# Optimization experiments

Hardware: AMD Instinct MI355X
Metric: run time of the kernel (lower is better)

Reference implementation:

```python
import jax, jax.numpy as jnp
from jax import lax
import numpy as np

# ---- config (repo globals, scaled to a 112x112 feature map of a 448 image) ----
IMG, FEAT = 448, 112
PSTRIDE = IMG // FEAT  # 4 pixels per feature cell
RATIOS = [(16, 16), (12, 20), (20, 12),
          (24, 24), (20, 28), (28, 20),
          (32, 32), (24, 40), (40, 24), (28, 40), (40, 28), (28, 36), (36, 28)]
GROUPS = [(0, 3), (3, 6), (6, 13)]   # ratio groups per NMS scale
N_LIST = [2, 3, 2]
IOU_THRESHS = [0.25, 0.25, 0.25]
BATCH = 256
WINDOW_NUMS = [(FEAT - rh + 1) * (FEAT - rw + 1) for rh, rw in RATIOS]
TOTAL = sum(WINDOW_NUMS)             # 96981
PROPOSALN = sum(N_LIST)              # 7


def _coordinates():
    # Mirrors ComputeCoordinate: box = [x0,y0,x1,y1] in pixels, lefttop clipped to 0.
    parts = []
    for rh, rw in RATIOS:
        nr, nc = FEAT - rh + 1, FEAT - rw + 1
        xi = np.repeat(np.arange(nr), nc).astype(np.float32)
        yi = np.tile(np.arange(nc), nr).astype(np.float32)
        x0 = xi * PSTRIDE - 1.0
        y0 = yi * PSTRIDE - 1.0
        x1 = x0 + rh * PSTRIDE
        y1 = y0 + rw * PSTRIDE
        x0 = np.maximum(x0, 0.0)
        y0 = np.maximum(y0, 0.0)
        parts.append(np.stack([x0, y0, x1, y1], 1))
    return np.concatenate(parts, 0).astype(np.float32)  # (TOTAL, 4)


def setup_inputs() -> dict:
    key = jax.random.key(0)
    x = jax.random.normal(key, (BATCH, 1, FEAT, FEAT), jnp.float32)
    coords = jnp.asarray(_coordinates())
    return {"x": x, "coords": coords, "proposalN": PROPOSALN}


def _nms(scores, coords, n_pick, thresh):
    # Greedy NMS: repeatedly take best-scoring alive window, suppress IoU > thresh.
    # If everything is suppressed before n_pick picks, repeat the last pick (repo behavior).
    areas = (coords[:, 2] - coords[:, 0] + 1.0) * (coords[:, 3] - coords[:, 1] + 1.0)

    def step(state, _):
        alive, last = state
        any_alive = jnp.any(alive)
        idx = jnp.where(any_alive,
                        jnp.argmax(jnp.where(alive, scores, -jnp.inf)).astype(jnp.int32),
                        last)
        box = coords[idx]
        lt = jnp.maximum(coords[:, :2], box[:2])
        rb = jnp.minimum(coords[:, 2:], box[2:])
        w = rb[:, 0] - lt[:, 0] + 1.0
        h = rb[:, 1] - lt[:, 1] + 1.0
        inter = jnp.where((w < 0) | (h < 0), 0.0, w * h)
        iou = inter / (areas + areas[idx] - inter)
        keep = (alive & (iou <= thresh)).at[idx].set(False)
        return (jnp.where(any_alive, keep, alive), idx), idx

    init = (jnp.ones(scores.shape[0], bool), jnp.int32(0))
    return lax.scan(step, init, None, length=n_pick)[1]  # (n_pick,) int32


def _forward(x, coords):
    B = x.shape[0]
    # multiscale sliding-window average scores (AvgPool2d, stride 1, VALID)
    avgs = [lax.reduce_window(x, 0.0, lax.add, (1, 1, rh, rw), (1, 1, 1, 1), 'VALID')
            .reshape(B, -1) / float(rh * rw) for rh, rw in RATIOS]
    all_scores = jnp.concatenate(avgs, 1)  # (B, TOTAL)

    idx_parts = []
    for j, (g0, g1) in enumerate(GROUPS):
        s0 = int(sum(WINDOW_NUMS[:g0]))
        s1 = int(sum(WINDOW_NUMS[:g1]))
        cd = coords[s0:s1]
        nms_j = lambda s, cd=cd, j=j: _nms(s, cd, N_LIST[j], IOU_THRESHS[j])
        picks = jax.vmap(nms_j)(all_scores[:, s0:s1])  # (B, N_LIST[j])
        idx_parts.append(picks + s0)
    proposalN_indices = jnp.concatenate(idx_parts, 1)  # (B, PROPOSALN)
    proposalN_windows_scores = jnp.take_along_axis(all_scores, proposalN_indices, 1)
    window_scores = all_scores  # reshape(batch, -1) of all_scores
    return proposalN_indices, proposalN_windows_scores, window_scores


def reference(x, coords, proposalN):
    assert proposalN == PROPOSALN
    return _forward(x, coords)
```

## Files before the change

kernel.cpp:

```cpp
#include <hip/hip_runtime.h>
#include <math.h>
#include <limits.h>

namespace {
constexpr int kFeat = 112;
constexpr int kBatch = 256;
constexpr int kTotal = 96981;
constexpr int kStride = 116;
constexpr int kNT = 512;
constexpr int kRH[13] = {16,12,20,24,20,28,32,24,40,28,40,28,36};
constexpr int kRW[13] = {16,20,12,24,28,20,32,40,24,40,28,36,28};
constexpr int kOff[13] = {0,9409,18802,28195,36116,44021,51926,58487,64984,71481,77686,83891,90436};
constexpr int kNQY[13] = {25,24,26,23,22,24,21,19,23,19,22,20,22};
constexpr int kNQ[13]  = {2425,2424,2418,2047,2046,2040,1701,1691,1679,1615,1606,1700,1694};
constexpr int kNB[13]  = {38,38,38,32,32,32,27,27,27,26,26,27,27};
constexpr int kNBMax = 187;

constexpr int nb_sum(int RB, int RE) {
  int s = 0;
  for (int r = RB; r < RE; ++r) s += kNB[r];
  return s;
}
}

__device__ __forceinline__ float* pad_score(float* sat, int e) {
  return sat + (e / 3) * kStride + 113 + (e % 3);
}
__device__ __forceinline__ unsigned char* pad_local(float* sat, int e) {
  const int i = 4 * kNBMax + e;
  const int r = i / 12;
  return (unsigned char*)sat + r * (kStride * 4) + 113 * 4 + (i - r * 12);
}

struct NmsShared {
  float rs[kNT / 64];
  int   ri[kNT / 64];
  float shS; int shI;
  float pX0[3], pY0[3], pX1[3], pY1[3], pA[3];
};

__device__ __forceinline__ void block_argmax(float s, int i, NmsShared* ns) {
  __syncthreads();
#pragma unroll
  for (int off = 32; off > 0; off >>= 1) {
    const float s2 = __shfl_down(s, off, 64);
    const int   i2 = __shfl_down(i, off, 64);
    if (s2 > s || (s2 == s && i2 < i)) { s = s2; i = i2; }
  }
  const int wave = threadIdx.x >> 6;
  if ((threadIdx.x & 63) == 0) { ns->rs[wave] = s; ns->ri[wave] = i; }
  __syncthreads();
  if (threadIdx.x == 0) {
    float bs = ns->rs[0]; int bi = ns->ri[0];
#pragma unroll
    for (int w = 1; w < kNT / 64; ++w)
      if (ns->rs[w] > bs || (ns->rs[w] == bs && ns->ri[w] < bi)) { bs = ns->rs[w]; bi = ns->ri[w]; }
    ns->shS = bs; ns->shI = bi;
  }
  __syncthreads();
}

__device__ void build_sat(const float* __restrict__ xb, float* __restrict__ sat) {
  const int tid = threadIdx.x;
  for (int j = tid; j < kStride; j += kNT) sat[j] = 0.f;
  for (int r = tid; r < 113; r += kNT) sat[r * kStride] = 0.f;
  const float4* x4 = (const float4*)xb;
  for (int i = tid; i < (kFeat * kFeat) / 4; i += kNT) {
    const float4 v = x4[i];
    const int r = i / (kFeat / 4);
    const int c = (i - r * (kFeat / 4)) * 4;
    float* dst = sat + (r + 1) * kStride + c + 1;
    dst[0] = v.x; dst[1] = v.y; dst[2] = v.z; dst[3] = v.w;
  }
  __syncthreads();
  const int wave = tid >> 6, lane = tid & 63;
  for (int r = 1 + wave; r <= kFeat; r += kNT / 64) {
    float* row = sat + r * kStride;
    float v = row[1 + lane];
#pragma unroll
    for (int d = 1; d < 64; d <<= 1) { const float u = __shfl_up(v, d, 64); if (lane >= d) v += u; }
    row[1 + lane] = v;
    const float tot = __shfl(v, 63, 64);
    const int c = 65 + lane;
    float w = (c <= kFeat) ? row[c] : 0.f;
#pragma unroll
    for (int d = 1; d < 64; d <<= 1) { const float u = __shfl_up(w, d, 64); if (lane >= d) w += u; }
    if (c <= kFeat) row[c] = w + tot;
  }
  __syncthreads();
  const int seg = tid / kFeat;
  const int col = tid - seg * kFeat + 1;
  if (tid < 4 * kFeat) {
    const int r0 = seg * 28 + 1;
    float s = 0.f;
    for (int r = r0; r < r0 + 28; ++r) { s += sat[r * kStride + col]; sat[r * kStride + col] = s; }
  }
  __syncthreads();
  float off = 0.f;
  if (tid < 4 * kFeat && seg > 0) {
#pragma unroll
    for (int s2 = 1; s2 <= 3; ++s2)
      if (s2 <= seg) off += sat[(28 * s2) * kStride + col];
  }
  __syncthreads();
  if (tid < 4 * kFeat && seg > 0) {
    const int r0 = seg * 28 + 1;
    for (int r = r0; r < r0 + 28; ++r) sat[r * kStride + col] += off;
  }
  __syncthreads();
}

template<int RB, int RE>
__device__ __forceinline__ void decode_geom(int pi, float& x0, float& y0,
                                            float& x1, float& y1, float& a) {
  x0 = 0.f; y0 = 0.f; x1 = 0.f; y1 = 0.f; a = 0.f;
#pragma unroll
  for (int rr = RB; rr < RE; ++rr) {
    const int nr = kFeat - kRH[rr] + 1, nc = kFeat - kRW[rr] + 1;
    if (pi >= kOff[rr] && pi < kOff[rr] + nr * nc) {
      const int l = pi - kOff[rr];
      const int xi = l / nc, yi = l - xi * nc;
      const float x0u = xi * 4.0f - 1.0f, y0u = yi * 4.0f - 1.0f;
      x1 = x0u + kRH[rr] * 4.0f; y1 = y0u + kRW[rr] * 4.0f;
      x0 = fmaxf(x0u, 0.0f); y0 = fmaxf(y0u, 0.0f);
      a = (x1 - x0 + 1.0f) * (y1 - y0 + 1.0f);
    }
  }
}

template<int RB, int RE>
__device__ __forceinline__ void pick_store(float* sat, NmsShared* ns, int k, int slot,
                                           float* __restrict__ out_idx,
                                           float* __restrict__ out_sc, int b) {
  if (threadIdx.x == 0) {
    const int e = ns->shI;
    const int local = (int)*pad_local(sat, e);
    int gi = 0, ebase = 0;
#pragma unroll
    for (int rr = RB; rr < RE; ++rr) {
      if (e >= ebase && e < ebase + kNB[rr]) {
        const int nqy = kNQY[rr], nc = kFeat - kRW[rr] + 1;
        const int qb = (e - ebase) << 6;
        const int bxi = qb / nqy;
        gi = kOff[rr] + bxi * nc + ((qb - bxi * nqy) << 2) + local;
      }
      ebase += kNB[rr];
    }
    float x0, y0, x1, y1, a;
    decode_geom<RB, RE>(gi, x0, y0, x1, y1, a);
    ns->pX0[k] = x0; ns->pY0[k] = y0; ns->pX1[k] = x1; ns->pY1[k] = y1; ns->pA[k] = a;
    out_idx[b * 7 + slot + k] = (float)gi;
    out_sc [b * 7 + slot + k] = ns->shS;
  }
  __syncthreads();
}

template<int RB, int RE, int NP, int SLOT>
__device__ void run_group(float* sat, NmsShared* ns,
                          float* __restrict__ wb,
                          float* __restrict__ out_idx, float* __restrict__ out_sc, int b) {
  constexpr int NBtot = nb_sum(RB, RE);
  const int tid = threadIdx.x;
  const int lane = tid & 63;
  const int wave = tid >> 6;

  int eb = 0;
#pragma unroll
  for (int rr = RB; rr < RE; ++rr) {
    const int rh = kRH[rr], rw = kRW[rr];
    const int nc = kFeat - rw + 1;
    const int nqy = kNQY[rr];
    const int NQ = kNQ[rr];
    const float inv = 1.0f / (float)(rh * rw);
    for (int qb = (tid & ~63); qb < NQ; qb += kNT) {
      const int q = qb + lane;
      const bool act = q < NQ;
      const int qc = act ? q : NQ - 1;
      const int xi = qc / nqy, qy = qc - xi * nqy;
      const int yi0 = qy << 2;
      const float* u = sat + xi * kStride;
      const float* d = u + rh * kStride;
      const float4 U0 = *(const float4*)(u + yi0);
      const float4 U1 = *(const float4*)(u + yi0 + rw);
      const float4 D0 = *(const float4*)(d + yi0);
      const float4 D1 = *(const float4*)(d + yi0 + rw);
      const float s0 = (D1.x - U1.x - D0.x + U0.x) * inv;
      const float s1 = (D1.y - U1.y - D0.y + U0.y) * inv;
      const float s2 = (D1.z - U1.z - D0.z + U0.z) * inv;
      const float s3 = (D1.w - U1.w - D0.w + U0.w) * inv;
      const int gi0 = kOff[rr] + xi * nc + yi0;
      const int rem = nc - yi0;
      float bs = -INFINITY; int bgi = INT_MAX;
      if (act) {
        float* w = wb + gi0;
        w[0] = s0; bs = s0; bgi = gi0;
        if (rem > 1) { w[1] = s1; if (s1 > bs) { bs = s1; bgi = gi0 + 1; } }
        if (rem > 2) { w[2] = s2; if (s2 > bs) { bs = s2; bgi = gi0 + 2; } }
        if (rem > 3) { w[3] = s3; if (s3 > bs) { bs = s3; bgi = gi0 + 3; } }
      }
      float wm = bs;
#pragma unroll
      for (int off = 32; off > 0; off >>= 1) wm = fmaxf(wm, __shfl_down(wm, off, 64));
      wm = __shfl(wm, 0, 64);
      const unsigned long long bal = __ballot(bs == wm);
      if (lane == __ffsll(bal) - 1) {
        const int e = eb + (qb >> 6);
        const int bxi = qb / nqy;
        const int giBase = kOff[rr] + bxi * nc + ((qb - bxi * nqy) << 2);
        *pad_score(sat, e) = wm;
        *pad_local(sat, e) = (unsigned char)(bgi - giBase);
      }
    }
    eb += kNB[rr];
  }
  __syncthreads();

  {
    const float s = (tid < NBtot) ? *pad_score(sat, tid) : -INFINITY;
    const int   i = (tid < NBtot) ? tid : INT_MAX;
    block_argmax(s, i, ns);
  }
  pick_store<RB, RE>(sat, ns, 0, SLOT, out_idx, out_sc, b);

  for (int k = 1; k < NP; ++k) {
    const float nx0 = ns->pX0[k-1], ny0 = ns->pY0[k-1];
    const float nx1 = ns->pX1[k-1], ny1 = ns->pY1[k-1], na = ns->pA[k-1];
    for (int e = wave; e < NBtot; e += kNT / 64) {
      const float es = *pad_score(sat, e);
      if (es == -INFINITY) continue;
      const int local = (int)*pad_local(sat, e);
      float x0 = 0.f, y0 = 0.f, x1 = 0.f, y1 = 0.f, a = 0.f;
      int eb2 = 0;
#pragma unroll
      for (int rr = RB; rr < RE; ++rr) {
        if (e >= eb2 && e < eb2 + kNB[rr]) {
          const int nqy = kNQY[rr], nc = kFeat - kRW[rr] + 1;
          const int qb2 = (e - eb2) << 6;
          const int bxi = qb2 / nqy;
          const int gi = kOff[rr] + bxi * nc + ((qb2 - bxi * nqy) << 2) + local;
          const int l = gi - kOff[rr];
          const int xi2 = l / nc, yi2 = l - xi2 * nc;
          const float x0u = xi2 * 4.0f - 1.0f, y0u = yi2 * 4.0f - 1.0f;
          x1 = x0u + kRH[rr] * 4.0f; y1 = y0u + kRW[rr] * 4.0f;
          x0 = fmaxf(x0u, 0.0f); y0 = fmaxf(y0u, 0.0f);
          a = (x1 - x0 + 1.0f) * (y1 - y0 + 1.0f);
        }
        eb2 += kNB[rr];
      }
      const float twx = fminf(x1, nx1) - fmaxf(x0, nx0) + 1.0f;
      const float thy = fminf(y1, ny1) - fmaxf(y0, ny0) + 1.0f;
      const bool sup = (twx >= 0.0f) & (thy >= 0.0f) & (5.0f * twx * thy > a + na);
      if (!sup) continue;
      int ebase = 0;
#pragma unroll
      for (int rr = RB; rr < RE; ++rr) {
        if (e >= ebase && e < ebase + kNB[rr]) {
          const int rh = kRH[rr], rw = kRW[rr];
          const int nc = kFeat - rw + 1;
          const int nqy = kNQY[rr];
          const int NQ = kNQ[rr];
          const float inv = 1.0f / (float)(rh * rw);
          const int q = ((e - ebase) << 6) + lane;
          const bool act = q < NQ;
          const int qc = act ? q : NQ - 1;
          const int xi = qc / nqy, qy = qc - xi * nqy;
          const int yi0 = qy << 2;
          const float* u = sat + xi * kStride;
          const float* d = u + rh * kStride;
          const float4 U0 = *(const float4*)(u + yi0);
          const float4 U1 = *(const float4*)(u + yi0 + rw);
          const float4 D0 = *(const float4*)(d + yi0);
          const float4 D1 = *(const float4*)(d + yi0 + rw);
          float s4[4];
          s4[0] = (D1.x - U1.x - D0.x + U0.x) * inv;
          s4[1] = (D1.y - U1.y - D0.y + U0.y) * inv;
          s4[2] = (D1.z - U1.z - D0.z + U0.z) * inv;
          s4[3] = (D1.w - U1.w - D0.w + U0.w) * inv;
          const float X0u = xi * 4.0f - 1.0f;
          const float X1 = X0u + rh * 4.0f;
          const float X0 = fmaxf(X0u, 0.0f);
          const float Ax = X1 - X0 + 1.0f;
          float wxp[NP > 1 ? NP - 1 : 1];
#pragma unroll
          for (int p = 0; p < NP - 1; ++p)
            if (p < k) wxp[p] = fminf(X1, ns->pX1[p]) - fmaxf(X0, ns->pX0[p]) + 1.0f;
          const int gi0 = kOff[rr] + xi * nc + yi0;
          const int rem = nc - yi0;
          float bs = -INFINITY; int bgi = INT_MAX;
          if (act) {
#pragma unroll
            for (int j = 0; j < 4; ++j) {
              if (j >= rem) break;
              const float Y0u = (yi0 + j) * 4.0f - 1.0f;
              const float Y1 = Y0u + rw * 4.0f;
              const float Y0 = fmaxf(Y0u, 0.0f);
              const float A = Ax * (Y1 - Y0 + 1.0f);
              bool alive = true;
#pragma unroll
              for (int p = 0; p < NP - 1; ++p) {
                if (p >= k) break;
                const float hyp = fminf(Y1, ns->pY1[p]) - fmaxf(Y0, ns->pY0[p]) + 1.0f;
                alive &= !((wxp[p] >= 0.0f) & (hyp >= 0.0f) &
                           (5.0f * wxp[p] * hyp > A + ns->pA[p]));
              }
              if (alive && s4[j] > bs) { bs = s4[j]; bgi = gi0 + j; }
            }
          }
          float wm = bs;
#pragma unroll
          for (int off = 32; off > 0; off >>= 1) wm = fmaxf(wm, __shfl_down(wm, off, 64));
          wm = __shfl(wm, 0, 64);
          const unsigned long long bal = __ballot(bs == wm);
          if (lane == __ffsll(bal) - 1) {
            const int qbB = (e - ebase) << 6;
            const int bxiB = qbB / nqy;
            const int giBase = kOff[rr] + bxiB * nc + ((qbB - bxiB * nqy) << 2);
            *pad_score(sat, e) = wm;
            *pad_local(sat, e) =
                (unsigned char)((bgi == INT_MAX) ? 0 : (bgi - giBase));
          }
        }
        ebase += kNB[rr];
      }
    }
    __syncthreads();
    {
      const float s = (tid < NBtot) ? *pad_score(sat, tid) : -INFINITY;
      const int   i = (tid < NBtot) ? tid : INT_MAX;
      block_argmax(s, i, ns);
    }
    pick_store<RB, RE>(sat, ns, k, SLOT, out_idx, out_sc, b);
  }
}

__global__ __launch_bounds__(kNT, 6) void appm_fused(const float* __restrict__ x,
                                                     float* __restrict__ win,
                                                     float* __restrict__ out_idx,
                                                     float* __restrict__ out_sc) {
  __shared__ __align__(16) float sat[113 * kStride];
  __shared__ NmsShared ns;
  const int b = blockIdx.x / 3;
  const int t = blockIdx.x % 3;

  build_sat(x + (size_t)b * kFeat * kFeat, sat);

  float* wb = win + (size_t)b * kTotal;
  if (t == 0)       run_group<0, 3, 2, 0>(sat, &ns, wb, out_idx, out_sc, b);
  else if (t == 1)  run_group<3, 6, 3, 2>(sat, &ns, wb, out_idx, out_sc, b);
  else              run_group<6, 13, 2, 5>(sat, &ns, wb, out_idx, out_sc, b);
}

extern "C" void kernel_launch(void* const* d_in, const int* in_sizes, int n_in,
                              void* d_out, int out_size, void* d_ws, size_t ws_size,
                              hipStream_t stream) {
  const float* x = (const float*)d_in[0];
  float* out     = (float*)d_out;
  float* out_idx = out;
  float* out_sc  = out + kBatch * 7;
  float* win     = out + 2 * kBatch * 7;

  appm_fused<<<kBatch * 3, kNT, 0, stream>>>(x, win, out_idx, out_sc);
}
```

Baseline: 175.4 us.

## Compute NMS dirty-block mask in parallel and round-robin rescans across waves

Before, each wave walked its own strided set of block entries and checked suppression one entry at a time. Now every thread tests one entry's suppression at once and publishes a per-wave ballot mask to shared memory. The dirty entries are then dealt round-robin across the eight waves for rescanning, so rescan work is balanced instead of depending on which wave owns which entry. This adds one barrier and a serial bitmask walk in every wave.

New measurement: 164.3 us. 6.3% less time.

```diff
diff --git a/kernel.cpp b/kernel.cpp
--- a/kernel.cpp
+++ b/kernel.cpp
@@ -37,6 +37,7 @@
   int   ri[kNT / 64];
   float shS; int shI;
   float pX0[3], pY0[3], pX1[3], pY1[3], pA[3];
+  unsigned long long dirtyM[kNT / 64];
 };
 
 __device__ __forceinline__ void block_argmax(float s, int i, NmsShared* ns) {
@@ -129,6 +130,30 @@
 }
 
 template<int RB, int RE>
+__device__ __forceinline__ void entry_geom(float* sat, int e, float& x0, float& y0,
+                                           float& x1, float& y1, float& a) {
+  const int local = (int)*pad_local(sat, e);
+  x0 = 0.f; y0 = 0.f; x1 = 0.f; y1 = 0.f; a = 0.f;
+  int eb = 0;
+#pragma unroll
+  for (int rr = RB; rr < RE; ++rr) {
+    if (e >= eb && e < eb + kNB[rr]) {
+      const int nqy = kNQY[rr], nc = kFeat - kRW[rr] + 1;
+      const int qb = (e - eb) << 6;
+      const int bxi = qb / nqy;
+      const int gi = kOff[rr] + bxi * nc + ((qb - bxi * nqy) << 2) + local;
+      const int l = gi - kOff[rr];
+      const int xi = l / nc, yi = l - xi * nc;
+      const float x0u = xi * 4.0f - 1.0f, y0u = yi * 4.0f - 1.0f;
+      x1 = x0u + kRH[rr] * 4.0f; y1 = y0u + kRW[rr] * 4.0f;
+      x0 = fmaxf(x0u, 0.0f); y0 = fmaxf(y0u, 0.0f);
+      a = (x1 - x0 + 1.0f) * (y1 - y0 + 1.0f);
+    }
+    eb += kNB[rr];
+  }
+}
+
+template<int RB, int RE>
 __device__ __forceinline__ void pick_store(float* sat, NmsShared* ns, int k, int slot,
                                            float* __restrict__ out_idx,
                                            float* __restrict__ out_sc, int b) {
@@ -153,6 +178,82 @@
     out_sc [b * 7 + slot + k] = ns->shS;
   }
   __syncthreads();
+}
+
+template<int RB, int RE, int NP>
+__device__ __forceinline__ void rescan_block(float* sat, NmsShared* ns, int e, int k,
+                                             int lane) {
+  int ebase = 0;
+#pragma unroll
+  for (int rr = RB; rr < RE; ++rr) {
+    if (e >= ebase && e < ebase + kNB[rr]) {
+      const int rh = kRH[rr], rw = kRW[rr];
+      const int nc = kFeat - rw + 1;
+      const int nqy = kNQY[rr];
+      const int NQ = kNQ[rr];
+      const float inv = 1.0f / (float)(rh * rw);
+      const int q = ((e - ebase) << 6) + lane;
+      const bool act = q < NQ;
+      const int qc = act ? q : NQ - 1;
+      const int xi = qc / nqy, qy = qc - xi * nqy;
+      const int yi0 = qy << 2;
+      const float* u = sat + xi * kStride;
+      const float* d = u + rh * kStride;
+      const float4 U0 = *(const float4*)(u + yi0);
+      const float4 U1 = *(const float4*)(u + yi0 + rw);
+      const float4 D0 = *(const float4*)(d + yi0);
+      const float4 D1 = *(const float4*)(d + yi0 + rw);
+      float s4[4];
+      s4[0] = (D1.x - U1.x - D0.x + U0.x) * inv;
+      s4[1] = (D1.y - U1.y - D0.y + U0.y) * inv;
+      s4[2] = (D1.z - U1.z - D0.z + U0.z) * inv;
+      s4[3] = (D1.w - U1.w - D0.w + U0.w) * inv;
+      const float X0u = xi * 4.0f - 1.0f;
+      const float X1 = X0u + rh * 4.0f;
+      const float X0 = fmaxf(X0u, 0.0f);
+      const float Ax = X1 - X0 + 1.0f;
+      float wxp[NP > 1 ? NP - 1 : 1];
+#pragma unroll
+      for (int p = 0; p < NP - 1; ++p)
+        if (p < k) wxp[p] = fminf(X1, ns->pX1[p]) - fmaxf(X0, ns->pX0[p]) + 1.0f;
+      const int gi0 = kOff[rr] + xi * nc + yi0;
+      const int rem = nc - yi0;
+      float bs = -INFINITY; int bgi = INT_MAX;
+      if (act) {
+#pragma unroll
+        for (int j = 0; j < 4; ++j) {
+          if (j >= rem) break;
+          const float Y0u = (yi0 + j) * 4.0f - 1.0f;
+          const float Y1 = Y0u + rw * 4.0f;
+          const float Y0 = fmaxf(Y0u, 0.0f);
+          const float A = Ax * (Y1 - Y0 + 1.0f);
+          bool alive = true;
+#pragma unroll
+          for (int p = 0; p < NP - 1; ++p) {
+            if (p >= k) break;
+            const float hyp = fminf(Y1, ns->pY1[p]) - fmaxf(Y0, ns->pY0[p]) + 1.0f;
+            alive &= !((wxp[p] >= 0.0f) & (hyp >= 0.0f) &
+                       (5.0f * wxp[p] * hyp > A + ns->pA[p]));
+          }
+          if (alive && s4[j] > bs) { bs = s4[j]; bgi = gi0 + j; }
+        }
+      }
+      float wm = bs;
+#pragma unroll
+      for (int off = 32; off > 0; off >>= 1) wm = fmaxf(wm, __shfl_down(wm, off, 64));
+      wm = __shfl(wm, 0, 64);
+      const unsigned long long bal = __ballot(bs == wm);
+      if (lane == __ffsll(bal) - 1) {
+        const int qbB = (e - ebase) << 6;
+        const int bxiB = qbB / nqy;
+        const int giBase = kOff[rr] + bxiB * nc + ((qbB - bxiB * nqy) << 2);
+        *pad_score(sat, e) = wm;
+        *pad_local(sat, e) =
+            (unsigned char)((bgi == INT_MAX) ? 0 : (bgi - giBase));
+      }
+    }
+    ebase += kNB[rr];
+  }
 }
 
 template<int RB, int RE, int NP, int SLOT>
@@ -225,105 +326,37 @@
   for (int k = 1; k < NP; ++k) {
     const float nx0 = ns->pX0[k-1], ny0 = ns->pY0[k-1];
     const float nx1 = ns->pX1[k-1], ny1 = ns->pY1[k-1], na = ns->pA[k-1];
-    for (int e = wave; e < NBtot; e += kNT / 64) {
-      const float es = *pad_score(sat, e);
-      if (es == -INFINITY) continue;
-      const int local = (int)*pad_local(sat, e);
-      float x0 = 0.f, y0 = 0.f, x1 = 0.f, y1 = 0.f, a = 0.f;
-      int eb2 = 0;
-#pragma unroll
-      for (int rr = RB; rr < RE; ++rr) {
-        if (e >= eb2 && e < eb2 + kNB[rr]) {
-          const int nqy = kNQY[rr], nc = kFeat - kRW[rr] + 1;
-          const int qb2 = (e - eb2) << 6;
-          const int bxi = qb2 / nqy;
-          const int gi = kOff[rr] + bxi * nc + ((qb2 - bxi * nqy) << 2) + local;
-          const int l = gi - kOff[rr];
-          const int xi2 = l / nc, yi2 = l - xi2 * nc;
-          const float x0u = xi2 * 4.0f - 1.0f, y0u = yi2 * 4.0f - 1.0f;
-          x1 = x0u + kRH[rr] * 4.0f; y1 = y0u + kRW[rr] * 4.0f;
-          x0 = fmaxf(x0u, 0.0f); y0 = fmaxf(y0u, 0.0f);
-          a = (x1 - x0 + 1.0f) * (y1 - y0 + 1.0f);
+
+    bool sup = false;
+    if (tid < NBtot) {
+      const float es = *pad_score(sat, tid);
+      if (es != -INFINITY) {
+        float x0, y0, x1, y1, a;
+        entry_geom<RB, RE>(sat, tid, x0, y0, x1, y1, a);
+        const float twx = fminf(x1, nx1) - fmaxf(x0, nx0) + 1.0f;
+        const float thy = fminf(y1, ny1) - fmaxf(y0, ny0) + 1.0f;
+        sup = (twx >= 0.0f) & (thy >= 0.0f) & (5.0f * twx * thy > a + na);
+      }
+    }
+    const unsigned long long m0 = __ballot(sup);
+    if (lane == 0) ns->dirtyM[wave] = m0;
+    __syncthreads();
+
+    int cnt = 0;
+#pragma unroll
+    for (int wm = 0; wm < kNT / 64; ++wm) {
+      unsigned long long m = ns->dirtyM[wm];
+      while (m) {
+        const int bit = __ffsll(m) - 1;
+        m &= m - 1;
+        if ((cnt & 7) == wave) {
+          rescan_block<RB, RE, NP>(sat, ns, (wm << 6) + bit, k, lane);
         }
-        eb2 += kNB[rr];
-      }
-      const float twx = fminf(x1, nx1) - fmaxf(x0, nx0) + 1.0f;
-      const float thy = fminf(y1, ny1) - fmaxf(y0, ny0) + 1.0f;
-      const bool sup = (twx >= 0.0f) & (thy >= 0.0f) & (5.0f * twx * thy > a + na);
-      if (!sup) continue;
-      int ebase = 0;
-#pragma unroll
-      for (int rr = RB; rr < RE; ++rr) {
-        if (e >= ebase && e < ebase + kNB[rr]) {
-          const int rh = kRH[rr], rw = kRW[rr];
-          const int nc = kFeat - rw + 1;
-          const int nqy = kNQY[rr];
-          const int NQ = kNQ[rr];
-          const float inv = 1.0f / (float)(rh * rw);
-          const int q = ((e - ebase) << 6) + lane;
-          const bool act = q < NQ;
-          const int qc = act ? q : NQ - 1;
-          const int xi = qc / nqy, qy = qc - xi * nqy;
-          const int yi0 = qy << 2;
-          const float* u = sat + xi * kStride;
-          const float* d = u + rh * kStride;
-          const float4 U0 = *(const float4*)(u + yi0);
-          const float4 U1 = *(const float4*)(u + yi0 + rw);
-          const float4 D0 = *(const float4*)(d + yi0);
-          const float4 D1 = *(const float4*)(d + yi0 + rw);
-          float s4[4];
-          s4[0] = (D1.x - U1.x - D0.x + U0.x) * inv;
-          s4[1] = (D1.y - U1.y - D0.y + U0.y) * inv;
-          s4[2] = (D1.z - U1.z - D0.z + U0.z) * inv;
-          s4[3] = (D1.w - U1.w - D0.w + U0.w) * inv;
-          const float X0u = xi * 4.0f - 1.0f;
-          const float X1 = X0u + rh * 4.0f;
-          const float X0 = fmaxf(X0u, 0.0f);
-          const float Ax = X1 - X0 + 1.0f;
-          float wxp[NP > 1 ? NP - 1 : 1];
-#pragma unroll
-          for (int p = 0; p < NP - 1; ++p)
-            if (p < k) wxp[p] = fminf(X1, ns->pX1[p]) - fmaxf(X0, ns->pX0[p]) + 1.0f;
-          const int gi0 = kOff[rr] + xi * nc + yi0;
-          const int rem = nc - yi0;
-          float bs = -INFINITY; int bgi = INT_MAX;
-          if (act) {
-#pragma unroll
-            for (int j = 0; j < 4; ++j) {
-              if (j >= rem) break;
-              const float Y0u = (yi0 + j) * 4.0f - 1.0f;
-              const float Y1 = Y0u + rw * 4.0f;
-              const float Y0 = fmaxf(Y0u, 0.0f);
-              const float A = Ax * (Y1 - Y0 + 1.0f);
-              bool alive = true;
-#pragma unroll
-              for (int p = 0; p < NP - 1; ++p) {
-                if (p >= k) break;
-                const float hyp = fminf(Y1, ns->pY1[p]) - fmaxf(Y0, ns->pY0[p]) + 1.0f;
-                alive &= !((wxp[p] >= 0.0f) & (hyp >= 0.0f) &
-                           (5.0f * wxp[p] * hyp > A + ns->pA[p]));
-              }
-              if (alive && s4[j] > bs) { bs = s4[j]; bgi = gi0 + j; }
-            }
-          }
-          float wm = bs;
-#pragma unroll
-          for (int off = 32; off > 0; off >>= 1) wm = fmaxf(wm, __shfl_down(wm, off, 64));
-          wm = __shfl(wm, 0, 64);
-          const unsigned long long bal = __ballot(bs == wm);
-          if (lane == __ffsll(bal) - 1) {
-            const int qbB = (e - ebase) << 6;
-            const int bxiB = qbB / nqy;
-            const int giBase = kOff[rr] + bxiB * nc + ((qbB - bxiB * nqy) << 2);
-            *pad_score(sat, e) = wm;
-            *pad_local(sat, e) =
-                (unsigned char)((bgi == INT_MAX) ? 0 : (bgi - giBase));
-          }
-        }
-        ebase += kNB[rr];
+        ++cnt;
       }
     }
     __syncthreads();
+
     {
       const float s = (tid < NBtot) ? *pad_score(sat, tid) : -INFINITY;
       const int   i = (tid < NBtot) ? tid : INT_MAX;
```
